# Optimization experiments

Hardware: AMD Instinct MI355X
Metric: run time of the kernel (lower is better)

The kernel has to match this reference:

```python
import jax, jax.numpy as jnp
import numpy as np


def log_g(x):
    # log of g(x) = where(x>=0, x+0.5, sigmoid(x))
    return jnp.where(x >= 0, jnp.log(jax.nn.relu(x) + 0.5), -jax.nn.softplus(-x))


def heinsen_scan_log(log_coeffs, log_values):
    # associative scan in log space over seq dim (axis=1)
    a_star = jnp.cumsum(log_coeffs, axis=1)
    log_h0_plus_b_star = jax.lax.cumlogsumexp(log_values - a_star, axis=1)
    return jnp.exp(a_star + log_h0_plus_b_star)


def setup_inputs() -> dict:
    key = jax.random.key(0)
    k1, k2, k3 = jax.random.split(key, 3)
    B, S, D_IN, D_INNER, D_OUT = 4, 4096, 1024, 1024, 1024
    x = jax.random.normal(k1, (B, S, D_IN), dtype=jnp.float32)
    # xavier_normal for Linear(d_in, 2*d_inner): std = sqrt(2/(fan_in+fan_out))
    std_hg = float(np.sqrt(2.0 / (D_IN + 2 * D_INNER)))
    W_hg = jax.random.normal(k2, (2 * D_INNER, D_IN), dtype=jnp.float32) * std_hg
    std_out = float(np.sqrt(2.0 / (D_INNER + D_OUT)))
    W_out = jax.random.normal(k3, (D_OUT, D_INNER), dtype=jnp.float32) * std_out
    return {"x": x, "W_hg": W_hg, "W_out": W_out}


def reference(x, W_hg, W_out):
    # x: [B,S,Din]; W_hg: [2*Dinner, Din]; W_out: [Dout, Dinner]
    hg = jnp.einsum("bsd,ed->bse", x, W_hg)
    hidden, gate = jnp.split(hg, 2, axis=-1)
    log_coeffs = -jax.nn.softplus(gate)        # log(1 - z)
    log_z = -jax.nn.softplus(-gate)            # log(z)
    log_values = log_z + log_g(hidden)
    h = heinsen_scan_log(log_coeffs, log_values)  # [B,S,Dinner]
    out = jnp.einsum("bsd,od->bso", h, W_out)
    return out
```

## Files before the change

### kernel.cpp

```cpp
#include <hip/hip_runtime.h>
#include <math.h>


typedef unsigned short ushort_t;
typedef unsigned int uint_t;
typedef __attribute__((ext_vector_type(4))) float f32x4;
typedef __attribute__((ext_vector_type(8))) __bf16 bf16x8;
typedef __attribute__((ext_vector_type(8))) unsigned short u16x8;

constexpr int Bsz  = 4;
constexpr int S    = 4096;
constexpr int Din  = 1024;
constexpr int Dh   = 1024;
constexpr int M    = Bsz * S;
constexpr int NCH  = 64;
constexpr int CL   = S / NCH;

__device__ __forceinline__ unsigned short f2bf(float f) {
    unsigned int u = __float_as_uint(f);
    unsigned int r = (u + 0x7fffu + ((u >> 16) & 1u)) >> 16;
    return (unsigned short)r;
}
__device__ __forceinline__ float bf2f(unsigned short u) {
    return __uint_as_float(((unsigned int)u) << 16);
}
__device__ __forceinline__ float sigf(float x) {
    x = fminf(fmaxf(x, -30.f), 30.f);
    return 1.0f / (1.0f + __expf(-x));
}
__device__ __forceinline__ void gld_lds16(const ushort_t* g, ushort_t* l) {
    __builtin_amdgcn_global_load_lds(
        (const __attribute__((address_space(1))) void*)g,
        (__attribute__((address_space(3))) void*)l, 16, 0, 0);
}

__global__ __launch_bounds__(256) void cvt_all(
    const float* __restrict__ x, const float* __restrict__ whg,
    const float* __restrict__ wout,
    ushort_t* __restrict__ xb, ushort_t* __restrict__ whgb,
    ushort_t* __restrict__ woutb)
{
    constexpr int NX = M * Din / 8;
    constexpr int NW = 2048 * 1024 / 8;
    const int i = blockIdx.x * 256 + threadIdx.x;
    const float* src; ushort_t* dst; int k;
    if (i < NX)            { src = x;    dst = xb;    k = i; }
    else if (i < NX + NW)  { src = whg;  dst = whgb;  k = i - NX; }
    else                   { src = wout; dst = woutb; k = i - NX - NW; }
    const float4 a = ((const float4*)src)[(size_t)k * 2];
    const float4 b = ((const float4*)src)[(size_t)k * 2 + 1];
    u16x8 o;
    o[0] = f2bf(a.x); o[1] = f2bf(a.y); o[2] = f2bf(a.z); o[3] = f2bf(a.w);
    o[4] = f2bf(b.x); o[5] = f2bf(b.y); o[6] = f2bf(b.z); o[7] = f2bf(b.w);
    ((u16x8*)dst)[k] = o;
}

__global__ __launch_bounds__(512, 2) void gemm256(
    const ushort_t* __restrict__ A, int lda,
    const ushort_t* __restrict__ B, int ldb,
    ushort_t* __restrict__ Cout, int ldc, int K, int nbx_log2)
{
    __shared__ ushort_t lds[4][2][8192];

    const int P = K >> 5;

    const int nwg = gridDim.x;
    const int cpx = nwg >> 3;
    const int bid = blockIdx.x;
    const int swz = (bid & 7) * cpx + (bid >> 3);
    const int bx  = swz & ((1 << nbx_log2) - 1);
    const int by  = swz >> nbx_log2;
    const int bm0 = by * 256;
    const int bn0 = bx * 256;

    const int t  = threadIdx.x;
    const int w  = t >> 6;
    const int l  = t & 63;
    const int wr = w >> 2;
    const int wc = w & 3;

    const int fr = l & 15;
    const int kg = l >> 4;
    const int qp = kg ^ (((fr >> 3) & 1) << 1);
    const int a_base = wr * 4096 + fr * 32 + qp * 8;
    const int b_base = wc * 2048 + fr * 32 + qp * 8;

    const int rs = l >> 2;
    const int lq = (l & 3) ^ (((rs >> 3) & 1) << 1);
    const ushort_t* gA0 = A + (size_t)(bm0 + w * 16 + rs) * lda + lq * 8;
    const ushort_t* gA1 = gA0 + (size_t)128 * lda;
    const ushort_t* gB0 = B + (size_t)(bn0 + w * 16 + rs) * ldb + lq * 8;
    const ushort_t* gB1 = gB0 + (size_t)128 * ldb;

    f32x4 acc[8][4];
    #pragma unroll
    for (int i = 0; i < 8; ++i)
        #pragma unroll
        for (int j = 0; j < 4; ++j)
            acc[i][j] = (f32x4){0.f, 0.f, 0.f, 0.f};

    auto stage = [&](int p) {
        const int s2 = p & 3;
        const int ko = p * 32;
        gld_lds16(gA0 + ko, &lds[s2][0][w * 512]);
        gld_lds16(gA1 + ko, &lds[s2][0][w * 512 + 4096]);
        gld_lds16(gB0 + ko, &lds[s2][1][w * 512]);
        gld_lds16(gB1 + ko, &lds[s2][1][w * 512 + 4096]);
    };

    auto phase_body = [&](int p, bool do_stage) {
        __builtin_amdgcn_s_barrier();
        __builtin_amdgcn_sched_barrier(0);
        const int s = p & 3;
        const ushort_t* la = &lds[s][0][0];
        const ushort_t* lb = &lds[s][1][0];
        bf16x8 af[8], bfr[4];
        #pragma unroll
        for (int i = 0; i < 8; ++i)
            af[i] = *reinterpret_cast<const bf16x8*>(&la[a_base + i * 512]);
        #pragma unroll
        for (int j = 0; j < 4; ++j)
            bfr[j] = *reinterpret_cast<const bf16x8*>(&lb[b_base + j * 512]);
        if (do_stage) stage(p + 2);
        __builtin_amdgcn_sched_barrier(0);
        __builtin_amdgcn_s_setprio(1);
        #pragma unroll
        for (int i = 0; i < 8; ++i)
            #pragma unroll
            for (int j = 0; j < 4; ++j)
                acc[i][j] = __builtin_amdgcn_mfma_f32_16x16x32_bf16(
                    af[i], bfr[j], acc[i][j], 0, 0, 0);
        __builtin_amdgcn_s_setprio(0);
        __builtin_amdgcn_sched_barrier(0);
    };

    stage(0);
    stage(1);

    for (int p = 0; p < P - 1; ++p) {
        asm volatile("s_waitcnt vmcnt(4)" ::: "memory");
        phase_body(p, p < P - 2);
    }
    asm volatile("s_waitcnt vmcnt(0)" ::: "memory");
    phase_body(P - 1, false);

    #pragma unroll
    for (int i = 0; i < 8; ++i) {
        #pragma unroll
        for (int j = 0; j < 4; ++j) {
            const int col = bn0 + wc * 64 + j * 16 + fr;
            #pragma unroll
            for (int r = 0; r < 4; ++r) {
                const int row = bm0 + wr * 128 + i * 16 + kg * 4 + r;
                Cout[(size_t)row * ldc + col] = f2bf(acc[i][j][r]);
            }
        }
    }
}

__global__ __launch_bounds__(512, 4) void gemm128(
    const ushort_t* __restrict__ A, int lda,
    const ushort_t* __restrict__ B, int ldb,
    float* __restrict__ Cout, int ldc, int K, int nbx_log2)
{
    __shared__ ushort_t lds[3][12288];

    const int P = K >> 5;

    const int nwg = gridDim.x;
    const int cpx = nwg >> 3;
    const int bid = blockIdx.x;
    const int swz = (bid & 7) * cpx + (bid >> 3);
    const int bx  = swz & ((1 << nbx_log2) - 1);
    const int by  = swz >> nbx_log2;
    const int bm0 = by * 128;
    const int bn0 = bx * 256;

    const int t  = threadIdx.x;
    const int w  = t >> 6;
    const int l  = t & 63;
    const int wr = w >> 2;
    const int wc = w & 3;

    const int fr = l & 15;
    const int kg = l >> 4;
    const int qp = kg ^ (((fr >> 3) & 1) << 1);
    const int a_base = wr * 2048 + fr * 32 + qp * 8;
    const int b_base = 4096 + wc * 2048 + fr * 32 + qp * 8;

    const int rs = l >> 2;
    const int lq = (l & 3) ^ (((rs >> 3) & 1) << 1);
    const ushort_t* gA0 = A + (size_t)(bm0 + w * 16 + rs) * lda + lq * 8;
    const ushort_t* gB0 = B + (size_t)(bn0 + w * 16 + rs) * ldb + lq * 8;
    const ushort_t* gB1 = gB0 + (size_t)128 * ldb;

    f32x4 acc[4][4];
    #pragma unroll
    for (int i = 0; i < 4; ++i)
        #pragma unroll
        for (int j = 0; j < 4; ++j)
            acc[i][j] = (f32x4){0.f, 0.f, 0.f, 0.f};

    auto stage = [&](int p, int s) {
        ushort_t* base = &lds[s][0];
        const int ko = p * 32;
        gld_lds16(gA0 + ko, base + w * 512);
        gld_lds16(gB0 + ko, base + 4096 + w * 512);
        gld_lds16(gB1 + ko, base + 8192 + w * 512);
    };

    stage(0, 0);
    stage(1, 1);

    int scur = 0;
    int snxt2 = 2;
    #pragma unroll 1
    for (int p = 0; p < P; ++p) {
        if (p < P - 1)
            asm volatile("s_waitcnt vmcnt(3)" ::: "memory");
        else
            asm volatile("s_waitcnt vmcnt(0)" ::: "memory");
        __builtin_amdgcn_s_barrier();
        __builtin_amdgcn_sched_barrier(0);
        const ushort_t* ls = &lds[scur][0];
        bf16x8 af[4], bfr[4];
        #pragma unroll
        for (int i = 0; i < 4; ++i)
            af[i] = *reinterpret_cast<const bf16x8*>(&ls[a_base + i * 512]);
        #pragma unroll
        for (int j = 0; j < 4; ++j)
            bfr[j] = *reinterpret_cast<const bf16x8*>(&ls[b_base + j * 512]);
        if (p + 2 < P) stage(p + 2, snxt2);
        __builtin_amdgcn_sched_barrier(0);
        __builtin_amdgcn_s_setprio(1);
        #pragma unroll
        for (int i = 0; i < 4; ++i)
            #pragma unroll
            for (int j = 0; j < 4; ++j)
                acc[i][j] = __builtin_amdgcn_mfma_f32_16x16x32_bf16(
                    af[i], bfr[j], acc[i][j], 0, 0, 0);
        __builtin_amdgcn_s_setprio(0);
        __builtin_amdgcn_sched_barrier(0);
        scur  = (scur  == 2) ? 0 : scur + 1;
        snxt2 = (snxt2 == 2) ? 0 : snxt2 + 1;
    }

    #pragma unroll
    for (int i = 0; i < 4; ++i) {
        #pragma unroll
        for (int j = 0; j < 4; ++j) {
            const int col = bn0 + wc * 64 + j * 16 + fr;
            #pragma unroll
            for (int r = 0; r < 4; ++r) {
                const int row = bm0 + wr * 64 + i * 16 + kg * 4 + r;
                Cout[(size_t)row * ldc + col] = acc[i][j][r];
            }
        }
    }
}

__global__ __launch_bounds__(256) void scan_fused(
    const ushort_t* __restrict__ hg, float* __restrict__ Apart,
    float* __restrict__ hlpart, int* __restrict__ flags,
    ushort_t* __restrict__ hout)
{
    const int bid   = blockIdx.x;
    const int half  = bid & 1;
    const int chunk = (bid >> 1) & (NCH - 1);
    const int b     = bid >> 7;
    const int t     = threadIdx.x;
    const int d     = half * 512 + 2 * t;
    const size_t rowbase = (size_t)(b * S + chunk * CL) * 2048 + d;

    float h0 = 0.f, h1 = 0.f, A0 = 1.f, A1 = 1.f;
    #pragma unroll 4
    for (int i = 0; i < CL; ++i) {
        const ushort_t* rp = hg + rowbase + (size_t)i * 2048;
        const uint_t hp = *(const uint_t*)rp;
        const uint_t gp = *(const uint_t*)(rp + 1024);
        const float hid0 = bf2f((ushort_t)hp), hid1 = bf2f((ushort_t)(hp >> 16));
        const float g0 = bf2f((ushort_t)gp),  g1 = bf2f((ushort_t)(gp >> 16));
        const float c0 = sigf(-g0), z0 = 1.f - c0;
        const float c1 = sigf(-g1), z1 = 1.f - c1;
        const float gv0 = (hid0 >= 0.f) ? (hid0 + 0.5f) : sigf(hid0);
        const float gv1 = (hid1 >= 0.f) ? (hid1 + 0.5f) : sigf(hid1);
        h0 = fmaf(c0, h0, z0 * gv0);  A0 *= c0;
        h1 = fmaf(c1, h1, z1 * gv1);  A1 *= c1;
    }

    const size_t pb = (size_t)(b * NCH + chunk) * 1024 + d;
    __hip_atomic_store(&Apart[pb],      A0, __ATOMIC_RELAXED, __HIP_MEMORY_SCOPE_AGENT);
    __hip_atomic_store(&Apart[pb + 1],  A1, __ATOMIC_RELAXED, __HIP_MEMORY_SCOPE_AGENT);
    __hip_atomic_store(&hlpart[pb],     h0, __ATOMIC_RELAXED, __HIP_MEMORY_SCOPE_AGENT);
    __hip_atomic_store(&hlpart[pb + 1], h1, __ATOMIC_RELAXED, __HIP_MEMORY_SCOPE_AGENT);
    __syncthreads();
    const int frow = (b * 2 + half) * NCH;
    if (t == 0) {
        __threadfence();
        __hip_atomic_store(&flags[frow + chunk], 1,
                           __ATOMIC_RELEASE, __HIP_MEMORY_SCOPE_AGENT);
    }

    while (!__syncthreads_and(
        (t >= chunk) ||
        __hip_atomic_load(&flags[frow + t], __ATOMIC_ACQUIRE,
                          __HIP_MEMORY_SCOPE_AGENT) != 0)) {
        __builtin_amdgcn_s_sleep(2);
    }

    float p0 = 0.f, p1 = 0.f;
    #pragma unroll 4
    for (int j = 0; j < chunk; ++j) {
        const size_t jb = (size_t)(b * NCH + j) * 1024 + d;
        const float Aj0 = __hip_atomic_load(&Apart[jb],      __ATOMIC_RELAXED, __HIP_MEMORY_SCOPE_AGENT);
        const float Aj1 = __hip_atomic_load(&Apart[jb + 1],  __ATOMIC_RELAXED, __HIP_MEMORY_SCOPE_AGENT);
        const float hj0 = __hip_atomic_load(&hlpart[jb],     __ATOMIC_RELAXED, __HIP_MEMORY_SCOPE_AGENT);
        const float hj1 = __hip_atomic_load(&hlpart[jb + 1], __ATOMIC_RELAXED, __HIP_MEMORY_SCOPE_AGENT);
        p0 = fmaf(Aj0, p0, hj0);
        p1 = fmaf(Aj1, p1, hj1);
    }

    const size_t hb = (size_t)(b * S + chunk * CL) * 1024 + d;
    h0 = p0; h1 = p1;
    #pragma unroll 4
    for (int i = 0; i < CL; ++i) {
        const ushort_t* rp = hg + rowbase + (size_t)i * 2048;
        const uint_t hp = *(const uint_t*)rp;
        const uint_t gp = *(const uint_t*)(rp + 1024);
        const float hid0 = bf2f((ushort_t)hp), hid1 = bf2f((ushort_t)(hp >> 16));
        const float g0 = bf2f((ushort_t)gp),  g1 = bf2f((ushort_t)(gp >> 16));
        const float c0 = sigf(-g0), z0 = 1.f - c0;
        const float c1 = sigf(-g1), z1 = 1.f - c1;
        const float gv0 = (hid0 >= 0.f) ? (hid0 + 0.5f) : sigf(hid0);
        const float gv1 = (hid1 >= 0.f) ? (hid1 + 0.5f) : sigf(hid1);
        h0 = fmaf(c0, h0, z0 * gv0);
        h1 = fmaf(c1, h1, z1 * gv1);
        const uint_t o = (uint_t)f2bf(h0) | ((uint_t)f2bf(h1) << 16);
        *(uint_t*)(hout + hb + (size_t)i * 1024) = o;
    }
}

extern "C" void kernel_launch(void* const* d_in, const int* in_sizes, int n_in,
                              void* d_out, int out_size, void* d_ws, size_t ws_size,
                              hipStream_t stream)
{
    (void)in_sizes; (void)n_in; (void)out_size; (void)ws_size;
    const float* x    = (const float*)d_in[0];
    const float* Whg  = (const float*)d_in[1];
    const float* Wout = (const float*)d_in[2];
    float* out = (float*)d_out;

    ushort_t* hgbuf = (ushort_t*)d_ws;
    ushort_t* xb    = hgbuf + (size_t)M * 2048;
    ushort_t* whgb  = xb + (size_t)M * 1024;
    ushort_t* woutb = whgb + (size_t)2048 * 1024;
    float*    Apart = (float*)(woutb + (size_t)1024 * 1024);
    float*    hlprt = Apart + (size_t)Bsz * NCH * Dh;
    int*      flags = (int*)(hlprt + (size_t)Bsz * NCH * Dh);

    const dim3 blk(256);

    hipMemsetAsync(flags, 0, Bsz * 2 * NCH * sizeof(int), stream);

    cvt_all<<<dim3(9728), blk, 0, stream>>>(x, Whg, Wout, xb, whgb, woutb);

    gemm256<<<dim3(512), dim3(512), 0, stream>>>(
        xb, Din, whgb, Din, hgbuf, 2048, Din, 3);

    scan_fused<<<dim3(512), blk, 0, stream>>>(hgbuf, Apart, hlprt, flags, xb);

    gemm128<<<dim3(512), dim3(512), 0, stream>>>(
        xb, Dh, woutb, Din, out, 1024, Dh, 2);
}
```

Baseline: 245.3 us.

## Split fused chunked scan into three kernels instead of flag-based inter-block sync

Replaces the single scan kernel that used global flags and spin-waiting for the cross-chunk carry with three launches. The first computes per-chunk decay products and local states, the second serially scans the 64 chunk carries per channel, and the third replays each chunk from its carry and writes bf16 hidden states. This removes the spin-wait, the memset and the quadratic per-block prefix reload. The cost is two extra kernel launches and a small serial stage-2 kernel with only 16 blocks.

```diff
diff --git a/kernel.cpp b/kernel.cpp
--- a/kernel.cpp
+++ b/kernel.cpp
@@ -259,10 +259,10 @@
     }
 }
 
-__global__ __launch_bounds__(256) void scan_fused(
-    const ushort_t* __restrict__ hg, float* __restrict__ Apart,
-    float* __restrict__ hlpart, int* __restrict__ flags,
-    ushort_t* __restrict__ hout)
+
+__global__ __launch_bounds__(256) void scan_stage1(
+    const ushort_t* __restrict__ hg, float* __restrict__ Abuf,
+    float* __restrict__ hlbuf)
 {
     const int bid   = blockIdx.x;
     const int half  = bid & 1;
@@ -287,41 +287,41 @@
         h0 = fmaf(c0, h0, z0 * gv0);  A0 *= c0;
         h1 = fmaf(c1, h1, z1 * gv1);  A1 *= c1;
     }
-
     const size_t pb = (size_t)(b * NCH + chunk) * 1024 + d;
-    __hip_atomic_store(&Apart[pb],      A0, __ATOMIC_RELAXED, __HIP_MEMORY_SCOPE_AGENT);
-    __hip_atomic_store(&Apart[pb + 1],  A1, __ATOMIC_RELAXED, __HIP_MEMORY_SCOPE_AGENT);
-    __hip_atomic_store(&hlpart[pb],     h0, __ATOMIC_RELAXED, __HIP_MEMORY_SCOPE_AGENT);
-    __hip_atomic_store(&hlpart[pb + 1], h1, __ATOMIC_RELAXED, __HIP_MEMORY_SCOPE_AGENT);
-    __syncthreads();
-    const int frow = (b * 2 + half) * NCH;
-    if (t == 0) {
-        __threadfence();
-        __hip_atomic_store(&flags[frow + chunk], 1,
-                           __ATOMIC_RELEASE, __HIP_MEMORY_SCOPE_AGENT);
-    }
-
-    while (!__syncthreads_and(
-        (t >= chunk) ||
-        __hip_atomic_load(&flags[frow + t], __ATOMIC_ACQUIRE,
-                          __HIP_MEMORY_SCOPE_AGENT) != 0)) {
-        __builtin_amdgcn_s_sleep(2);
-    }
-
-    float p0 = 0.f, p1 = 0.f;
-    #pragma unroll 4
-    for (int j = 0; j < chunk; ++j) {
-        const size_t jb = (size_t)(b * NCH + j) * 1024 + d;
-        const float Aj0 = __hip_atomic_load(&Apart[jb],      __ATOMIC_RELAXED, __HIP_MEMORY_SCOPE_AGENT);
-        const float Aj1 = __hip_atomic_load(&Apart[jb + 1],  __ATOMIC_RELAXED, __HIP_MEMORY_SCOPE_AGENT);
-        const float hj0 = __hip_atomic_load(&hlpart[jb],     __ATOMIC_RELAXED, __HIP_MEMORY_SCOPE_AGENT);
-        const float hj1 = __hip_atomic_load(&hlpart[jb + 1], __ATOMIC_RELAXED, __HIP_MEMORY_SCOPE_AGENT);
-        p0 = fmaf(Aj0, p0, hj0);
-        p1 = fmaf(Aj1, p1, hj1);
-    }
-
-    const size_t hb = (size_t)(b * S + chunk * CL) * 1024 + d;
-    h0 = p0; h1 = p1;
+    *(float2*)&Abuf[pb]  = make_float2(A0, A1);
+    *(float2*)&hlbuf[pb] = make_float2(h0, h1);
+}
+
+__global__ __launch_bounds__(256) void scan_stage2(
+    const float* __restrict__ Abuf, const float* __restrict__ hlbuf,
+    float* __restrict__ Hs)
+{
+    const int g = blockIdx.x * 256 + threadIdx.x;
+    const int d = g & (Dh - 1);
+    const int b = g >> 10;
+    float h = 0.0f;
+    for (int ch = 0; ch < NCH; ++ch) {
+        const size_t o = (size_t)(b * NCH + ch) * Dh + d;
+        Hs[o] = h;
+        h = fmaf(Abuf[o], h, hlbuf[o]);
+    }
+}
+
+__global__ __launch_bounds__(256) void scan_stage3(
+    const ushort_t* __restrict__ hg, const float* __restrict__ Hs,
+    ushort_t* __restrict__ hout)
+{
+    const int bid   = blockIdx.x;
+    const int half  = bid & 1;
+    const int chunk = (bid >> 1) & (NCH - 1);
+    const int b     = bid >> 7;
+    const int t     = threadIdx.x;
+    const int d     = half * 512 + 2 * t;
+    const size_t rowbase = (size_t)(b * S + chunk * CL) * 2048 + d;
+    const size_t hb      = (size_t)(b * S + chunk * CL) * 1024 + d;
+
+    const float2 hs = *(const float2*)&Hs[(size_t)(b * NCH + chunk) * 1024 + d];
+    float h0 = hs.x, h1 = hs.y;
     #pragma unroll 4
     for (int i = 0; i < CL; ++i) {
         const ushort_t* rp = hg + rowbase + (size_t)i * 2048;
@@ -354,20 +354,20 @@
     ushort_t* xb    = hgbuf + (size_t)M * 2048;
     ushort_t* whgb  = xb + (size_t)M * 1024;
     ushort_t* woutb = whgb + (size_t)2048 * 1024;
-    float*    Apart = (float*)(woutb + (size_t)1024 * 1024);
-    float*    hlprt = Apart + (size_t)Bsz * NCH * Dh;
-    int*      flags = (int*)(hlprt + (size_t)Bsz * NCH * Dh);
+    float*    Abuf  = (float*)(woutb + (size_t)1024 * 1024);
+    float*    hlbuf = Abuf + (size_t)Bsz * NCH * Dh;
+    float*    Hsbuf = hlbuf + (size_t)Bsz * NCH * Dh;
 
     const dim3 blk(256);
-
-    hipMemsetAsync(flags, 0, Bsz * 2 * NCH * sizeof(int), stream);
 
     cvt_all<<<dim3(9728), blk, 0, stream>>>(x, Whg, Wout, xb, whgb, woutb);
 
     gemm256<<<dim3(512), dim3(512), 0, stream>>>(
         xb, Din, whgb, Din, hgbuf, 2048, Din, 3);
 
-    scan_fused<<<dim3(512), blk, 0, stream>>>(hgbuf, Apart, hlprt, flags, xb);
+    scan_stage1<<<dim3(512), blk, 0, stream>>>(hgbuf, Abuf, hlbuf);
+    scan_stage2<<<dim3(Bsz * Dh / 256), blk, 0, stream>>>(Abuf, hlbuf, Hsbuf);
+    scan_stage3<<<dim3(512), blk, 0, stream>>>(hgbuf, Hsbuf, xb);
 
     gemm128<<<dim3(512), dim3(512), 0, stream>>>(
         xb, Dh, woutb, Din, out, 1024, Dh, 2);
```

Measured after the change: 207.7 us. -15.4%, faster.
